# Optimization experiments

Measured on AMD Instinct MI355X. Metric: run time of the kernel, lower is better.

The kernel has to match this reference:

```python
import jax, jax.numpy as jnp
import numpy as np

NS = 8  # number of bins (init arg ns)


def setup_inputs() -> dict:
    key = jax.random.key(0)
    x = jax.random.normal(key, (16, 512, 128, 128), dtype=jnp.float32)
    return {"x": x}


def _make_hk(Hc, C, ns, height):
    """Sequential threshold binning: per batch row, scan j and record bin edges.

    Hc: [B, height] exclusive cumulative counts of per-(b,c) argmax rows.
    Returns hks: [B, ns+1] float32 with hks[:,0]=0, hks[:,ns]=height.
    """

    def row_fn(hrow):
        hks0 = jnp.zeros(ns + 1, jnp.float32).at[ns].set(float(height))

        def step(carry, j):
            k, hks = carry
            t = ((k * C) // ns).astype(hrow.dtype)  # int(k*C/ns)
            cond = (k < ns) & (hrow[j] <= t) & (hrow[j + 1] > t)
            hks = hks.at[k].set(jnp.where(cond, j.astype(jnp.float32), hks[k]))
            k = k + cond.astype(k.dtype)
            return (k, hks), None

        # original loop: j in [1, height-2] (breaks when j+1 >= height)
        js = jnp.arange(1, height - 1, dtype=jnp.int32)
        (_, hks), _ = jax.lax.scan(step, (jnp.int32(1), hks0), js)
        return hks

    return jax.vmap(row_fn)(Hc)


def _forward(x, ns):
    B, C, H, W = x.shape
    a = x.reshape(B, C, H * W)
    vmax = jnp.max(a, axis=2, keepdims=True)
    # argmax indicator mask (ties all set to 1, matching a == max)
    I = (a == vmax).astype(x.dtype).reshape(B, C, H, W)
    # per-row counts of argmax positions, summed over channels & width: [B, H]
    rc = I.sum(axis=(1, 3))
    # H[:, i] = sum of I over rows < i  -> exclusive cumulative sum
    Hc = jnp.concatenate(
        [jnp.zeros((B, 1), x.dtype), jnp.cumsum(rc, axis=1)[:, :-1]], axis=1
    )
    hk = _make_hk(Hc, C, ns, H)  # [B, ns+1]
    F = x.sum(axis=(2, 3)) / W  # [B, C]
    hk_sub = hk[:, 1:] - hk[:, :-1]  # [B, ns]
    # F repeated over ns bins, divided by bin widths, flattened: [B, ns*C]
    return (F[:, None, :] / hk_sub[:, :, None]).reshape(B, ns * C)


def reference(x):
    return _forward(x, NS)
```

## Files before the change

kernel.cpp:

```cpp
#include <hip/hip_runtime.h>

#define Bdim 16
#define Cdim 512
#define Hdim 128
#define Wdim 128
#define NS 8

__global__ __launch_bounds__(256) void chan_reduce(const float* __restrict__ x,
                                                   int* __restrict__ rc,
                                                   float* __restrict__ F) {
    const int bid = blockIdx.x;
    const int tid = threadIdx.x;
    const float4* __restrict__ p = (const float4*)(x + ((size_t)bid << 14));

    float4 r[16];
    float tmax = -INFINITY;
    float tsum = 0.f;
#pragma unroll
    for (int i = 0; i < 16; ++i) {
        r[i] = p[i * 256 + tid];
        tsum += (r[i].x + r[i].y) + (r[i].z + r[i].w);
        tmax = fmaxf(tmax, fmaxf(fmaxf(r[i].x, r[i].y), fmaxf(r[i].z, r[i].w)));
    }

#pragma unroll
    for (int off = 32; off > 0; off >>= 1) {
        tsum += __shfl_down(tsum, off, 64);
        tmax = fmaxf(tmax, __shfl_down(tmax, off, 64));
    }

    __shared__ float smax[4], ssum[4];
    const int wave = tid >> 6;
    if ((tid & 63) == 0) { smax[wave] = tmax; ssum[wave] = tsum; }
    __syncthreads();

    const float bmax = fmaxf(fmaxf(smax[0], smax[1]), fmaxf(smax[2], smax[3]));
    if (tid == 0) {
        F[bid] = (ssum[0] + ssum[1] + ssum[2] + ssum[3]) * (1.0f / Wdim);
    }

    const int b = bid >> 9;
    const int rsub = tid >> 5;
#pragma unroll
    for (int i = 0; i < 16; ++i) {
        int cnt = (r[i].x == bmax) + (r[i].y == bmax) +
                  (r[i].z == bmax) + (r[i].w == bmax);
        if (cnt) atomicAdd(&rc[b * Hdim + i * 8 + rsub], cnt);
    }
}

__global__ __launch_bounds__(256) void finalize(const int* __restrict__ rc,
                                                const float* __restrict__ F,
                                                float* __restrict__ out) {
    const int b = blockIdx.x;
    const int tid = threadIdx.x;
    __shared__ int s_rc[Hdim];
    __shared__ int s_Hc[Hdim + 1];
    __shared__ float s_sub[NS];

    if (tid < Hdim) s_rc[tid] = rc[b * Hdim + tid];
    __syncthreads();

    if (tid == 0) {
        s_Hc[0] = 0;
        for (int i = 1; i <= Hdim; ++i) s_Hc[i] = s_Hc[i - 1] + s_rc[i - 1];
        float hks[NS + 1];
        for (int k = 0; k <= NS; ++k) hks[k] = 0.f;
        hks[NS] = (float)Hdim;
        int k = 1;
        for (int j = 1; j <= Hdim - 2; ++j) {
            int t = (k * Cdim) / NS;
            if (k < NS && s_Hc[j] <= t && s_Hc[j + 1] > t) {
                hks[k] = (float)j;
                ++k;
            }
        }
        for (int q = 0; q < NS; ++q) s_sub[q] = hks[q + 1] - hks[q];
    }
    __syncthreads();

    for (int idx = tid; idx < NS * Cdim; idx += 256) {
        int k = idx >> 9;
        int c = idx & (Cdim - 1);
        out[b * (NS * Cdim) + idx] = F[b * Cdim + c] / s_sub[k];
    }
}

extern "C" void kernel_launch(void* const* d_in, const int* in_sizes, int n_in,
                              void* d_out, int out_size, void* d_ws, size_t ws_size,
                              hipStream_t stream) {
    const float* x = (const float*)d_in[0];
    float* out = (float*)d_out;
    int* rc = (int*)d_ws;
    float* F = (float*)((char*)d_ws + Bdim * Hdim * sizeof(int));

    hipMemsetAsync(rc, 0, Bdim * Hdim * sizeof(int), stream);
    chan_reduce<<<Bdim * Cdim, 256, 0, stream>>>(x, rc, F);
    finalize<<<Bdim, 256, 0, stream>>>(rc, F, out);
}
```

Before: 685.5 us.

## Assign one wave per channel and stream data with compact argmax bitmasks

Each wavefront now reduces a whole channel on its own, which removes the shared-memory exchange and block barrier. Instead of keeping 64 floats per thread in registers, it streams the data with nontemporal loads and records per-chunk max bitmasks and packed tie counts. Atomics are issued only for chunks whose max equals the channel max. This lowers register pressure so more waves can be resident while staying bandwidth-bound. The cost is more bookkeeping ALU work and a different atomic row mapping that has to stay consistent with the row layout.

```diff
diff --git a/kernel.cpp b/kernel.cpp
--- a/kernel.cpp
+++ b/kernel.cpp
@@ -6,47 +6,75 @@
 #define Wdim 128
 #define NS 8
 
+typedef float vfloat4 __attribute__((ext_vector_type(4)));
+
 __global__ __launch_bounds__(256) void chan_reduce(const float* __restrict__ x,
                                                    int* __restrict__ rc,
                                                    float* __restrict__ F) {
-    const int bid = blockIdx.x;
     const int tid = threadIdx.x;
-    const float4* __restrict__ p = (const float4*)(x + ((size_t)bid << 14));
+    const int lane = tid & 63;
+    const int ch = blockIdx.x * 4 + (tid >> 6);
+    const int b = ch >> 9;
+    const vfloat4* __restrict__ p = (const vfloat4*)(x + ((size_t)ch << 14)) + lane;
 
-    float4 r[16];
+    float tsum = 0.f;
     float tmax = -INFINITY;
-    float tsum = 0.f;
-#pragma unroll
-    for (int i = 0; i < 16; ++i) {
-        r[i] = p[i * 256 + tid];
-        tsum += (r[i].x + r[i].y) + (r[i].z + r[i].w);
-        tmax = fmaxf(tmax, fmaxf(fmaxf(r[i].x, r[i].y), fmaxf(r[i].z, r[i].w)));
+    unsigned mask0, mask1, mask2, mask3;
+    unsigned cpk0, cpk1, cpk2, cpk3;
+    float cm0, cm1, cm2, cm3;
+
+#define CHUNK(cc, MASK, CPK, CMX)                                              \
+    {                                                                          \
+        unsigned m = 0, cp = 0;                                                \
+        float chmax = -INFINITY;                                               \
+        _Pragma("unroll") for (int i = 0; i < 16; ++i) {                       \
+            const vfloat4 v = __builtin_nontemporal_load(&p[(cc * 16 + i) * 64]); \
+            const float mx = fmaxf(fmaxf(v[0], v[1]), fmaxf(v[2], v[3]));      \
+            const int c = (v[0] == mx) + (v[1] == mx) + (v[2] == mx) + (v[3] == mx); \
+            cp |= (unsigned)(c - 1) << (2 * i);                                \
+            const unsigned bit = 1u << i;                                      \
+            const bool gt = mx > chmax;                                        \
+            const bool eq = mx == chmax;                                       \
+            m = gt ? bit : (m | (eq ? bit : 0u));                              \
+            chmax = fmaxf(chmax, mx);                                          \
+            tsum += (v[0] + v[1]) + (v[2] + v[3]);                             \
+        }                                                                      \
+        MASK = m; CPK = cp; CMX = chmax;                                       \
+        tmax = fmaxf(tmax, chmax);                                             \
     }
 
+    CHUNK(0, mask0, cpk0, cm0)
+    CHUNK(1, mask1, cpk1, cm1)
+    CHUNK(2, mask2, cpk2, cm2)
+    CHUNK(3, mask3, cpk3, cm3)
+#undef CHUNK
+
+    float wsum = tsum, wmax = tmax;
 #pragma unroll
     for (int off = 32; off > 0; off >>= 1) {
-        tsum += __shfl_down(tsum, off, 64);
-        tmax = fmaxf(tmax, __shfl_down(tmax, off, 64));
+        wsum += __shfl_xor(wsum, off, 64);
+        wmax = fmaxf(wmax, __shfl_xor(wmax, off, 64));
     }
 
-    __shared__ float smax[4], ssum[4];
-    const int wave = tid >> 6;
-    if ((tid & 63) == 0) { smax[wave] = tmax; ssum[wave] = tsum; }
-    __syncthreads();
+    if (lane == 0) F[ch] = wsum * (1.0f / Wdim);
 
-    const float bmax = fmaxf(fmaxf(smax[0], smax[1]), fmaxf(smax[2], smax[3]));
-    if (tid == 0) {
-        F[bid] = (ssum[0] + ssum[1] + ssum[2] + ssum[3]) * (1.0f / Wdim);
+    const int rbase = b * Hdim + (lane >> 5);
+#define RECOUNT(cc, MASK, CPK, CMX)                                            \
+    if (CMX == wmax) {                                                         \
+        unsigned m = MASK;                                                     \
+        while (m) {                                                            \
+            const int i = __builtin_ctz(m);                                    \
+            m &= m - 1;                                                        \
+            atomicAdd(&rc[rbase + 2 * (cc * 16 + i)],                          \
+                      (int)((CPK >> (2 * i)) & 3u) + 1);                       \
+        }                                                                      \
     }
 
-    const int b = bid >> 9;
-    const int rsub = tid >> 5;
-#pragma unroll
-    for (int i = 0; i < 16; ++i) {
-        int cnt = (r[i].x == bmax) + (r[i].y == bmax) +
-                  (r[i].z == bmax) + (r[i].w == bmax);
-        if (cnt) atomicAdd(&rc[b * Hdim + i * 8 + rsub], cnt);
-    }
+    RECOUNT(0, mask0, cpk0, cm0)
+    RECOUNT(1, mask1, cpk1, cm1)
+    RECOUNT(2, mask2, cpk2, cm2)
+    RECOUNT(3, mask3, cpk3, cm3)
+#undef RECOUNT
 }
 
 __global__ __launch_bounds__(256) void finalize(const int* __restrict__ rc,
@@ -95,6 +123,6 @@
     float* F = (float*)((char*)d_ws + Bdim * Hdim * sizeof(int));
 
     hipMemsetAsync(rc, 0, Bdim * Hdim * sizeof(int), stream);
-    chan_reduce<<<Bdim * Cdim, 256, 0, stream>>>(x, rc, F);
+    chan_reduce<<<(Bdim * Cdim) / 4, 256, 0, stream>>>(x, rc, F);
     finalize<<<Bdim, 256, 0, stream>>>(rc, F, out);
 }
```

After: 689.9 us. No clear change (+0.6%).
